# Optimization experiments

Measured on AMD Instinct MI355X. Metric: run time of the kernel, lower is better.

Reference implementation:

```python
import jax, jax.numpy as jnp
import numpy as np

N_NODES = 50000
N_REL = 1000
N_EDGES = 600000
D = 128
DEPTH = 2


def setup_inputs() -> dict:
    key = jax.random.key(0)
    ks = jax.random.split(key, 10)
    features = jax.random.normal(ks[0], (N_NODES, D), dtype=jnp.float32)
    rel_emb = jax.random.normal(ks[1], (N_REL, D), dtype=jnp.float32)
    # edge list: row0 = destination (sorted, matches coalesced sparse layout), row1 = source
    dst = jnp.sort(jax.random.randint(ks[2], (N_EDGES,), 0, N_NODES))
    src = jax.random.randint(ks[3], (N_EDGES,), 0, N_NODES)
    adj = jnp.stack([dst, src]).astype(jnp.int64)
    # one relation entry per triple: r_index[0]=triple id, r_index[1]=relation id
    r_index = jnp.stack([
        jnp.arange(N_EDGES, dtype=jnp.int64),
        jax.random.randint(ks[4], (N_EDGES,), 0, N_REL).astype(jnp.int64),
    ])
    r_val = jax.random.uniform(ks[5], (N_EDGES,), dtype=jnp.float32)
    # Xavier-ish params
    attn_w = jax.random.normal(ks[6], (3 * D, 1), dtype=jnp.float32) * 0.05
    attn_b = jnp.zeros((1,), dtype=jnp.float32)
    gate_w = jax.random.normal(ks[7], (3 * D, 1), dtype=jnp.float32) * 0.05
    gate_b = jnp.zeros((1,), dtype=jnp.float32)
    attn_kernels = jax.random.normal(ks[8], (DEPTH, D, 1), dtype=jnp.float32) * (6.0 / (D + 1)) ** 0.5
    return {"features": features, "rel_emb": rel_emb, "adj": adj, "r_index": r_index,
            "r_val": r_val, "attn_w": attn_w, "attn_b": attn_b, "gate_w": gate_w,
            "gate_b": gate_b, "attn_kernels": attn_kernels}


def _segment_softmax(vals, seg, n):
    # numerically stable softmax over edges grouped by destination node `seg`
    m = jax.ops.segment_max(vals, seg, num_segments=n)
    e = jnp.exp(vals - m[seg])
    s = jax.ops.segment_sum(e, seg, num_segments=n)
    return e / s[seg]


def reference(features, rel_emb, adj, r_index, r_val, attn_w, attn_b, gate_w, gate_b, attn_kernels):
    n_nodes = features.shape[0]
    n_triples = adj.shape[1]
    depth = attn_kernels.shape[0]
    dst, src_idx = adj[0], adj[1]

    feats = jnp.tanh(features)
    outs_c = [feats]
    outs_s = [feats]

    for l in range(depth):
        # sparse [triple, rel] @ rel_emb -> per-triple relation embedding
        tri_rel = jax.ops.segment_sum(r_val[:, None] * rel_emb[r_index[1]], r_index[0],
                                      num_segments=n_triples)  # [E, D]
        tri_rel = tri_rel / jnp.maximum(
            jnp.linalg.norm(tri_rel, axis=1, keepdims=True), 1e-12)
        # gather neighbors and reflect through relation hyperplane
        neighs = feats[src_idx]  # [E, D]
        neighs = neighs - 2.0 * jnp.sum(neighs * tri_rel, axis=1, keepdims=True) * tri_rel
        # structural attention + row-wise sparse softmax
        att_struct = _segment_softmax((tri_rel @ attn_kernels[l])[:, 0], dst, n_nodes)
        feats = jnp.tanh(jax.ops.segment_sum(neighs * att_struct[:, None], dst,
                                             num_segments=n_nodes))
        outs_c.append(feats)
        # semantic branch on updated features
        neighs2 = feats[src_idx]
        source_emb = feats[dst]
        diff_raw = source_emb - neighs2
        att_input = jnp.concatenate([source_emb, neighs2, diff_raw], axis=-1)  # [E, 3D]
        att_score = jnp.maximum(jax.nn.sigmoid(att_input @ attn_w + attn_b)[:, 0], 1e-4)
        gate_score = jax.nn.sigmoid(att_input @ gate_w + gate_b)[:, 0]
        final_att = gate_score * att_score + (1.0 - gate_score) * att_struct
        att = _segment_softmax(final_att, dst, n_nodes)
        new_diff = jnp.tanh(jax.ops.segment_sum(diff_raw * att[:, None], dst,
                                                num_segments=n_nodes))
        outs_s.append(new_diff)

    return (jnp.concatenate(outs_c, axis=-1), jnp.concatenate(outs_s, axis=-1))
```

## Files before the change

kernel.cpp:

```cpp
#include <hip/hip_runtime.h>
#include <math.h>

#define N_NODES 50000
#define N_REL   1000
#define N_EDGES 600000
#define D       128
#define OUT_COLS 384

typedef unsigned short ushortT;

#define FEAT0_BLOCKS  ((N_NODES * (D / 4) + 255) / 256)
#define RELN_BLOCKS   ((N_REL + 3) / 4)
#define ROWPTR_BLOCKS ((N_NODES + 1 + 255) / 256)
#define SETUP_BLOCKS  (FEAT0_BLOCKS + RELN_BLOCKS + ROWPTR_BLOCKS + 1)

__device__ __forceinline__ float wave_reduce_sum64(float v) {
#pragma unroll
    for (int m = 1; m < 64; m <<= 1) v += __shfl_xor(v, m, 64);
    return v;
}

template <int CTRL>
__device__ __forceinline__ float dpp_add_(float v) {
    int t = __builtin_amdgcn_update_dpp(0, __float_as_int(v), CTRL, 0xf, 0xf, true);
    return v + __int_as_float(t);
}
__device__ __forceinline__ float group_sum16(float v) {
    v = dpp_add_<0xB1>(v);
    v = dpp_add_<0x4E>(v);
    v = dpp_add_<0x141>(v);
    v = dpp_add_<0x140>(v);
    return v;
}

__device__ __forceinline__ float tanh_fast(float x) {
    float cx = fminf(fmaxf(x, -20.0f), 20.0f);
    float e = __expf(2.0f * cx);
    return __fdividef(e - 1.0f, e + 1.0f);
}
__device__ __forceinline__ float sigmoid_fast(float x) {
    return __fdividef(1.0f, 1.0f + __expf(-x));
}

__device__ __forceinline__ void bf16x8_to_f32(uint4 q, float4& a, float4& b) {
    a.x = __int_as_float((int)(q.x << 16));
    a.y = __int_as_float((int)(q.x & 0xffff0000u));
    a.z = __int_as_float((int)(q.y << 16));
    a.w = __int_as_float((int)(q.y & 0xffff0000u));
    b.x = __int_as_float((int)(q.z << 16));
    b.y = __int_as_float((int)(q.z & 0xffff0000u));
    b.z = __int_as_float((int)(q.w << 16));
    b.w = __int_as_float((int)(q.w & 0xffff0000u));
}
__device__ __forceinline__ unsigned pack_bf16x2(float lo, float hi) {
    unsigned a = __float_as_uint(lo), b = __float_as_uint(hi);
    a = (a + 0x7fffu + ((a >> 16) & 1u)) >> 16;
    b = (b + 0x7fffu + ((b >> 16) & 1u));
    return (a & 0xffffu) | (b & 0xffff0000u);
}

__global__ __launch_bounds__(256) void k_setup(
        const float* __restrict__ features, const float* __restrict__ rel_emb,
        const float* __restrict__ attn_k, const float* __restrict__ attn_w,
        const float* __restrict__ gate_w, const int* __restrict__ dstv,
        float* __restrict__ out0, float* __restrict__ out1, ushortT* __restrict__ fc0,
        float* __restrict__ rel_norm, float* __restrict__ er0, float* __restrict__ er1,
        float* __restrict__ wcomb, int* __restrict__ row_ptr) {
    int bid = blockIdx.x, tid = threadIdx.x;
    if (bid < FEAT0_BLOCKS) {
        int i = bid * 256 + tid;
        if (i >= N_NODES * (D / 4)) return;
        int n = i >> 5, q = i & 31;
        float4 f = *(const float4*)(features + (size_t)n * D + 4 * q);
        f.x = tanh_fast(f.x); f.y = tanh_fast(f.y);
        f.z = tanh_fast(f.z); f.w = tanh_fast(f.w);
        *(float4*)(out0 + (size_t)n * OUT_COLS + 4 * q) = f;
        *(float4*)(out1 + (size_t)n * OUT_COLS + 4 * q) = f;
        uint2 p = make_uint2(pack_bf16x2(f.x, f.y), pack_bf16x2(f.z, f.w));
        *((uint2*)(fc0 + (size_t)n * D) + q) = p;
    } else if (bid < FEAT0_BLOCKS + RELN_BLOCKS) {
        int wid  = (bid - FEAT0_BLOCKS) * 4 + (tid >> 6);
        int lane = tid & 63;
        if (wid >= N_REL) return;
        float2 v = *(const float2*)(rel_emb + (size_t)wid * D + 2 * lane);
        float sq = wave_reduce_sum64(v.x * v.x + v.y * v.y);
        float inv = 1.0f / fmaxf(sqrtf(sq), 1e-12f);
        float2 u = make_float2(v.x * inv, v.y * inv);
        *(float2*)(rel_norm + (size_t)wid * D + 2 * lane) = u;
        float2 k0 = *(const float2*)(attn_k + 2 * lane);
        float2 k1 = *(const float2*)(attn_k + D + 2 * lane);
        float d0 = wave_reduce_sum64(u.x * k0.x + u.y * k0.y);
        float d1 = wave_reduce_sum64(u.x * k1.x + u.y * k1.y);
        if (lane == 0) { er0[wid] = __expf(d0); er1[wid] = __expf(d1); }
    } else if (bid < FEAT0_BLOCKS + RELN_BLOCKS + ROWPTR_BLOCKS) {
        int n = (bid - FEAT0_BLOCKS - RELN_BLOCKS) * 256 + tid;
        if (n > N_NODES) return;
        int lo = 0, hi = N_EDGES;
        while (lo < hi) {
            int mid = (lo + hi) >> 1;
            if (dstv[mid] < n) lo = mid + 1; else hi = mid;
        }
        row_ptr[n] = lo;
    } else {
        int j = tid;
        if (j >= D) return;
        wcomb[j]         = attn_w[j] + attn_w[2 * D + j];
        wcomb[D + j]     = attn_w[D + j] - attn_w[2 * D + j];
        wcomb[2 * D + j] = gate_w[j] + gate_w[2 * D + j];
        wcomb[3 * D + j] = gate_w[D + j] - gate_w[2 * D + j];
    }
}

__global__ __launch_bounds__(256) void k_struct(
        const ushortT* __restrict__ finC,
        ushortT* __restrict__ foutC,
        float* __restrict__ foutS,
        const int* __restrict__ row_ptr, const int* __restrict__ srcv,
        const int* __restrict__ relv, const float* __restrict__ rval,
        const float* __restrict__ er,
        const float* __restrict__ rel_norm, const float* __restrict__ wcomb,
        float* __restrict__ node_Z, float* __restrict__ proj) {
    int n    = (blockIdx.x * blockDim.x + threadIdx.x) >> 6;
    int lane = threadIdx.x & 63;
    int g = lane >> 4, l = lane & 15;
    if (n >= N_NODES) return;
    int beg = row_ptr[n], end = row_ptr[n + 1];

    float4 acc0 = make_float4(0.f, 0.f, 0.f, 0.f);
    float4 acc1 = make_float4(0.f, 0.f, 0.f, 0.f);
    float Zp = 0.f;

    for (int cs = beg; cs < end; cs += 64) {
        int cnt = min(64, end - cs);
        int my_s = 0, my_r = -1; float my_w = 0.f;
        if (lane < cnt) {
            int e = cs + lane;
            my_s = srcv[e];
            int rr = relv[e];
            bool pos = rval[e] > 0.0f;
            my_r = pos ? rr : -1;
            my_w = pos ? er[rr] : 1.0f;
            Zp += my_w;
        }
        int nit = (cnt + 3) >> 2;
        int   s = __shfl(my_s, g, 64);
        int   r = __shfl(my_r, g, 64);
        float w = __shfl(my_w, g, 64);
        uint4 xq = *((const uint4*)(finC + (size_t)s * D) + l);
        {
            int rr = r < 0 ? 0 : r;
            const float* up = rel_norm + (size_t)rr * D + 8 * l;
            float4 u0 = *(const float4*)up;
            float4 u1 = *(const float4*)(up + 4);
            for (int i = 0; i < nit; ++i) {
                int s_c = s; int r_c = r; float w_c = w;
                uint4 xq_c = xq; float4 u0_c = u0, u1_c = u1;
                (void)s_c;
                if (i + 1 < nit) {
                    int sl2 = ((i + 1) << 2) | g;
                    s = __shfl(my_s, sl2, 64);
                    r = __shfl(my_r, sl2, 64);
                    w = __shfl(my_w, sl2, 64);
                    xq = *((const uint4*)(finC + (size_t)s * D) + l);
                    int rr2 = r < 0 ? 0 : r;
                    const float* up2 = rel_norm + (size_t)rr2 * D + 8 * l;
                    u0 = *(const float4*)up2;
                    u1 = *(const float4*)(up2 + 4);
                }
                float4 x0, x1;
                bf16x8_to_f32(xq_c, x0, x1);
                float p = x0.x*u0_c.x + x0.y*u0_c.y + x0.z*u0_c.z + x0.w*u0_c.w
                        + x1.x*u1_c.x + x1.y*u1_c.y + x1.z*u1_c.z + x1.w*u1_c.w;
                p = group_sum16(p);
                float wc = (r_c >= 0) ? 2.0f * w_c * p : 0.0f;
                acc0.x += w_c * x0.x - wc * u0_c.x;
                acc0.y += w_c * x0.y - wc * u0_c.y;
                acc0.z += w_c * x0.z - wc * u0_c.z;
                acc0.w += w_c * x0.w - wc * u0_c.w;
                acc1.x += w_c * x1.x - wc * u1_c.x;
                acc1.y += w_c * x1.y - wc * u1_c.y;
                acc1.z += w_c * x1.z - wc * u1_c.z;
                acc1.w += w_c * x1.w - wc * u1_c.w;
            }
        }
    }
    float Z = group_sum16(Zp);
    Z += __shfl_xor(Z, 16, 64);
    Z += __shfl_xor(Z, 32, 64);
#pragma unroll
    for (int m = 16; m < 64; m <<= 1) {
        acc0.x += __shfl_xor(acc0.x, m, 64);
        acc0.y += __shfl_xor(acc0.y, m, 64);
        acc0.z += __shfl_xor(acc0.z, m, 64);
        acc0.w += __shfl_xor(acc0.w, m, 64);
        acc1.x += __shfl_xor(acc1.x, m, 64);
        acc1.y += __shfl_xor(acc1.y, m, 64);
        acc1.z += __shfl_xor(acc1.z, m, 64);
        acc1.w += __shfl_xor(acc1.w, m, 64);
    }
    float invZ = (end > beg) ? (1.0f / Z) : 0.0f;
    float4 o0, o1;
    o0.x = tanh_fast(acc0.x * invZ); o0.y = tanh_fast(acc0.y * invZ);
    o0.z = tanh_fast(acc0.z * invZ); o0.w = tanh_fast(acc0.w * invZ);
    o1.x = tanh_fast(acc1.x * invZ); o1.y = tanh_fast(acc1.y * invZ);
    o1.z = tanh_fast(acc1.z * invZ); o1.w = tanh_fast(acc1.w * invZ);

    float pr[4];
#pragma unroll
    for (int k = 0; k < 4; ++k) {
        const float* wp = wcomb + k * D + 8 * l;
        float4 w0 = *(const float4*)wp;
        float4 w1 = *(const float4*)(wp + 4);
        float p = o0.x*w0.x + o0.y*w0.y + o0.z*w0.z + o0.w*w0.w
                + o1.x*w1.x + o1.y*w1.y + o1.z*w1.z + o1.w*w1.w;
        pr[k] = group_sum16(p);
    }
    if (lane == 0) {
        node_Z[n] = Z;
        *(float4*)(proj + 4 * (size_t)n) = make_float4(pr[0], pr[1], pr[2], pr[3]);
    }
    if (g == 0) {
        float* op = foutS + (size_t)n * OUT_COLS + 8 * l;
        *(float4*)op = o0;
        *(float4*)(op + 4) = o1;
        uint4 pk = make_uint4(pack_bf16x2(o0.x, o0.y), pack_bf16x2(o0.z, o0.w),
                              pack_bf16x2(o1.x, o1.y), pack_bf16x2(o1.z, o1.w));
        *((uint4*)(foutC + (size_t)n * D) + l) = pk;
    }
}

__global__ __launch_bounds__(256) void k_sem(
        const ushortT* __restrict__ featsC,
        const float* __restrict__ seF,
        float* __restrict__ oput,
        const int* __restrict__ row_ptr, const int* __restrict__ srcv,
        const int* __restrict__ relv, const float* __restrict__ rval,
        const float* __restrict__ er, const float* __restrict__ node_Z,
        const float* __restrict__ proj,
        const float* __restrict__ attn_b, const float* __restrict__ gate_b) {
    int n    = (blockIdx.x * blockDim.x + threadIdx.x) >> 6;
    int lane = threadIdx.x & 63;
    int g = lane >> 4, l = lane & 15;
    if (n >= N_NODES) return;
    int beg = row_ptr[n], end = row_ptr[n + 1];

    float4 pn = *(const float4*)(proj + 4 * (size_t)n);
    float ca = pn.x + attn_b[0];
    float cg = pn.z + gate_b[0];
    float invZ = (end > beg) ? (1.0f / node_Z[n]) : 0.0f;

    float4 acc0 = make_float4(0.f, 0.f, 0.f, 0.f);
    float4 acc1 = make_float4(0.f, 0.f, 0.f, 0.f);
    float Zs = 0.f;

    for (int cs = beg; cs < end; cs += 64) {
        int cnt = min(64, end - cs);
        int my_s = 0; float my_wt = 0.f;
        if (lane < cnt) {
            int e = cs + lane;
            my_s = srcv[e];
            int rr = relv[e];
            bool pos = rval[e] > 0.0f;
            float sw = (pos ? er[rr] : 1.0f) * invZ;
            float4 ps = *(const float4*)(proj + 4 * (size_t)my_s);
            float as = fmaxf(sigmoid_fast(ca + ps.y), 1e-4f);
            float gt = sigmoid_fast(cg + ps.w);
            my_wt = __expf(gt * as + (1.0f - gt) * sw);
            Zs += my_wt;
        }
        int nit = (cnt + 3) >> 2;
        int   s  = __shfl(my_s, g, 64);
        float wt = __shfl(my_wt, g, 64);
        uint4 xq = *((const uint4*)(featsC + (size_t)s * D) + l);
        for (int i = 0; i < nit; ++i) {
            float wt_c = wt; uint4 xq_c = xq;
            if (i + 1 < nit) {
                int sl2 = ((i + 1) << 2) | g;
                s  = __shfl(my_s, sl2, 64);
                wt = __shfl(my_wt, sl2, 64);
                xq = *((const uint4*)(featsC + (size_t)s * D) + l);
            }
            float4 x0, x1;
            bf16x8_to_f32(xq_c, x0, x1);
            acc0.x += wt_c * x0.x; acc0.y += wt_c * x0.y;
            acc0.z += wt_c * x0.z; acc0.w += wt_c * x0.w;
            acc1.x += wt_c * x1.x; acc1.y += wt_c * x1.y;
            acc1.z += wt_c * x1.z; acc1.w += wt_c * x1.w;
        }
    }
    Zs = group_sum16(Zs);
    Zs += __shfl_xor(Zs, 16, 64);
    Zs += __shfl_xor(Zs, 32, 64);
#pragma unroll
    for (int m = 16; m < 64; m <<= 1) {
        acc0.x += __shfl_xor(acc0.x, m, 64);
        acc0.y += __shfl_xor(acc0.y, m, 64);
        acc0.z += __shfl_xor(acc0.z, m, 64);
        acc0.w += __shfl_xor(acc0.w, m, 64);
        acc1.x += __shfl_xor(acc1.x, m, 64);
        acc1.y += __shfl_xor(acc1.y, m, 64);
        acc1.z += __shfl_xor(acc1.z, m, 64);
        acc1.w += __shfl_xor(acc1.w, m, 64);
    }
    if (g == 0) {
        float invZs = (end > beg) ? (1.0f / Zs) : 0.0f;
        float sc    = (end > beg) ? 1.0f : 0.0f;
        const float* sp = seF + (size_t)n * OUT_COLS + 8 * l;
        float4 s0 = *(const float4*)sp;
        float4 s1 = *(const float4*)(sp + 4);
        float4 o0, o1;
        o0.x = tanh_fast(sc * (s0.x - acc0.x * invZs));
        o0.y = tanh_fast(sc * (s0.y - acc0.y * invZs));
        o0.z = tanh_fast(sc * (s0.z - acc0.z * invZs));
        o0.w = tanh_fast(sc * (s0.w - acc0.w * invZs));
        o1.x = tanh_fast(sc * (s1.x - acc1.x * invZs));
        o1.y = tanh_fast(sc * (s1.y - acc1.y * invZs));
        o1.z = tanh_fast(sc * (s1.z - acc1.z * invZs));
        o1.w = tanh_fast(sc * (s1.w - acc1.w * invZs));
        float* op = oput + (size_t)n * OUT_COLS + 8 * l;
        *(float4*)op = o0;
        *(float4*)(op + 4) = o1;
    }
}

extern "C" void kernel_launch(void* const* d_in, const int* in_sizes, int n_in,
                              void* d_out, int out_size, void* d_ws, size_t ws_size,
                              hipStream_t stream) {
    const float* features = (const float*)d_in[0];
    const float* rel_emb  = (const float*)d_in[1];
    const int*   adj      = (const int*)d_in[2];
    const int*   r_index  = (const int*)d_in[3];
    const float* r_val    = (const float*)d_in[4];
    const float* attn_w   = (const float*)d_in[5];
    const float* attn_b   = (const float*)d_in[6];
    const float* gate_w   = (const float*)d_in[7];
    const float* gate_b   = (const float*)d_in[8];
    const float* attn_k   = (const float*)d_in[9];

    float* out0 = (float*)d_out;
    float* out1 = out0 + (size_t)N_NODES * OUT_COLS;

    float* rel_norm = (float*)d_ws;
    float* er0      = rel_norm + (size_t)N_REL * D;
    float* er1      = er0 + N_REL;
    float* wcomb    = er1 + N_REL;
    float* proj     = wcomb + 4 * D;
    float* node_Z   = proj + 4 * (size_t)N_NODES;
    int*   row_ptr  = (int*)(node_Z + N_NODES);
    ushortT* fc0    = (ushortT*)(row_ptr + N_NODES + 4);
    ushortT* fc1    = fc0 + (size_t)N_NODES * D;
    ushortT* fc2    = fc1 + (size_t)N_NODES * D;

    const int* dstv = adj;
    const int* srcv = adj + N_EDGES;
    const int* relv = r_index + N_EDGES;

    k_setup<<<SETUP_BLOCKS, 256, 0, stream>>>(
        features, rel_emb, attn_k, attn_w, gate_w, dstv,
        out0, out1, fc0, rel_norm, er0, er1, wcomb, row_ptr);

    const ushortT* fcin[3] = {fc0, fc1, fc2};
    for (int l = 0; l < 2; ++l) {
        const float* er = l ? er1 : er0;
        k_struct<<<(N_NODES + 3) / 4, 256, 0, stream>>>(
            fcin[l], (ushortT*)fcin[l + 1], out0 + (size_t)(l + 1) * D,
            row_ptr, srcv, relv, r_val, er, rel_norm, wcomb, node_Z, proj);
        k_sem<<<(N_NODES + 3) / 4, 256, 0, stream>>>(
            fcin[l + 1], out0 + (size_t)(l + 1) * D, out1 + (size_t)(l + 1) * D,
            row_ptr, srcv, relv, r_val, er, node_Z, proj, attn_b, gate_b);
    }
}
```

Before: 376.9 us.

## Fuse layer-0 semantic pass with layer-1 structural pass into one kernel

New measurement: 360.6 us. -4.3%, faster.

```diff
diff --git a/kernel.cpp b/kernel.cpp
--- a/kernel.cpp
+++ b/kernel.cpp
@@ -147,41 +147,38 @@
         int   r = __shfl(my_r, g, 64);
         float w = __shfl(my_w, g, 64);
         uint4 xq = *((const uint4*)(finC + (size_t)s * D) + l);
-        {
-            int rr = r < 0 ? 0 : r;
-            const float* up = rel_norm + (size_t)rr * D + 8 * l;
-            float4 u0 = *(const float4*)up;
-            float4 u1 = *(const float4*)(up + 4);
-            for (int i = 0; i < nit; ++i) {
-                int s_c = s; int r_c = r; float w_c = w;
-                uint4 xq_c = xq; float4 u0_c = u0, u1_c = u1;
-                (void)s_c;
-                if (i + 1 < nit) {
-                    int sl2 = ((i + 1) << 2) | g;
-                    s = __shfl(my_s, sl2, 64);
-                    r = __shfl(my_r, sl2, 64);
-                    w = __shfl(my_w, sl2, 64);
-                    xq = *((const uint4*)(finC + (size_t)s * D) + l);
-                    int rr2 = r < 0 ? 0 : r;
-                    const float* up2 = rel_norm + (size_t)rr2 * D + 8 * l;
-                    u0 = *(const float4*)up2;
-                    u1 = *(const float4*)(up2 + 4);
-                }
-                float4 x0, x1;
-                bf16x8_to_f32(xq_c, x0, x1);
-                float p = x0.x*u0_c.x + x0.y*u0_c.y + x0.z*u0_c.z + x0.w*u0_c.w
-                        + x1.x*u1_c.x + x1.y*u1_c.y + x1.z*u1_c.z + x1.w*u1_c.w;
-                p = group_sum16(p);
-                float wc = (r_c >= 0) ? 2.0f * w_c * p : 0.0f;
-                acc0.x += w_c * x0.x - wc * u0_c.x;
-                acc0.y += w_c * x0.y - wc * u0_c.y;
-                acc0.z += w_c * x0.z - wc * u0_c.z;
-                acc0.w += w_c * x0.w - wc * u0_c.w;
-                acc1.x += w_c * x1.x - wc * u1_c.x;
-                acc1.y += w_c * x1.y - wc * u1_c.y;
-                acc1.z += w_c * x1.z - wc * u1_c.z;
-                acc1.w += w_c * x1.w - wc * u1_c.w;
+        int rr0 = r < 0 ? 0 : r;
+        const float* up = rel_norm + (size_t)rr0 * D + 8 * l;
+        float4 u0 = *(const float4*)up;
+        float4 u1 = *(const float4*)(up + 4);
+        for (int i = 0; i < nit; ++i) {
+            int r_c = r; float w_c = w;
+            uint4 xq_c = xq; float4 u0_c = u0, u1_c = u1;
+            if (i + 1 < nit) {
+                int sl2 = ((i + 1) << 2) | g;
+                s = __shfl(my_s, sl2, 64);
+                r = __shfl(my_r, sl2, 64);
+                w = __shfl(my_w, sl2, 64);
+                xq = *((const uint4*)(finC + (size_t)s * D) + l);
+                int rr2 = r < 0 ? 0 : r;
+                const float* up2 = rel_norm + (size_t)rr2 * D + 8 * l;
+                u0 = *(const float4*)up2;
+                u1 = *(const float4*)(up2 + 4);
             }
+            float4 x0, x1;
+            bf16x8_to_f32(xq_c, x0, x1);
+            float p = x0.x*u0_c.x + x0.y*u0_c.y + x0.z*u0_c.z + x0.w*u0_c.w
+                    + x1.x*u1_c.x + x1.y*u1_c.y + x1.z*u1_c.z + x1.w*u1_c.w;
+            p = group_sum16(p);
+            float wc = (r_c >= 0) ? 2.0f * w_c * p : 0.0f;
+            acc0.x += w_c * x0.x - wc * u0_c.x;
+            acc0.y += w_c * x0.y - wc * u0_c.y;
+            acc0.z += w_c * x0.z - wc * u0_c.z;
+            acc0.w += w_c * x0.w - wc * u0_c.w;
+            acc1.x += w_c * x1.x - wc * u1_c.x;
+            acc1.y += w_c * x1.y - wc * u1_c.y;
+            acc1.z += w_c * x1.z - wc * u1_c.z;
+            acc1.w += w_c * x1.w - wc * u1_c.w;
         }
     }
     float Z = group_sum16(Zp);
@@ -226,6 +223,164 @@
         uint4 pk = make_uint4(pack_bf16x2(o0.x, o0.y), pack_bf16x2(o0.z, o0.w),
                               pack_bf16x2(o1.x, o1.y), pack_bf16x2(o1.z, o1.w));
         *((uint4*)(foutC + (size_t)n * D) + l) = pk;
+    }
+}
+
+__global__ __launch_bounds__(256) void k_fused(
+        const ushortT* __restrict__ finC,
+        const float* __restrict__ seF,
+        ushortT* __restrict__ foutC,
+        float* __restrict__ foutS,
+        float* __restrict__ oputSem,
+        const int* __restrict__ row_ptr, const int* __restrict__ srcv,
+        const int* __restrict__ relv, const float* __restrict__ rval,
+        const float* __restrict__ er_sem,
+        const float* __restrict__ er_st,
+        const float* __restrict__ rel_norm, const float* __restrict__ wcomb,
+        const float* __restrict__ node_Z0, const float* __restrict__ proj0,
+        float* __restrict__ node_Z1, float* __restrict__ proj1,
+        const float* __restrict__ attn_b, const float* __restrict__ gate_b) {
+    int n    = (blockIdx.x * blockDim.x + threadIdx.x) >> 6;
+    int lane = threadIdx.x & 63;
+    int g = lane >> 4, l = lane & 15;
+    if (n >= N_NODES) return;
+    int beg = row_ptr[n], end = row_ptr[n + 1];
+
+    float4 pn = *(const float4*)(proj0 + 4 * (size_t)n);
+    float ca = pn.x + attn_b[0];
+    float cg = pn.z + gate_b[0];
+    float invZ0 = (end > beg) ? (1.0f / node_Z0[n]) : 0.0f;
+
+    float4 st0 = make_float4(0.f, 0.f, 0.f, 0.f);
+    float4 st1 = make_float4(0.f, 0.f, 0.f, 0.f);
+    float4 sm0 = make_float4(0.f, 0.f, 0.f, 0.f);
+    float4 sm1 = make_float4(0.f, 0.f, 0.f, 0.f);
+    float Zp = 0.f, Zs = 0.f;
+
+    for (int cs = beg; cs < end; cs += 64) {
+        int cnt = min(64, end - cs);
+        int my_s = 0, my_r = -1; float my_w = 0.f, my_wt = 0.f;
+        if (lane < cnt) {
+            int e = cs + lane;
+            my_s = srcv[e];
+            int rr = relv[e];
+            bool pos = rval[e] > 0.0f;
+            my_r = pos ? rr : -1;
+            my_w = pos ? er_st[rr] : 1.0f;
+            float sw = (pos ? er_sem[rr] : 1.0f) * invZ0;
+            float4 ps = *(const float4*)(proj0 + 4 * (size_t)my_s);
+            float as = fmaxf(sigmoid_fast(ca + ps.y), 1e-4f);
+            float gt = sigmoid_fast(cg + ps.w);
+            my_wt = __expf(gt * as + (1.0f - gt) * sw);
+            Zp += my_w; Zs += my_wt;
+        }
+        int nit = (cnt + 3) >> 2;
+        int   s  = __shfl(my_s, g, 64);
+        int   r  = __shfl(my_r, g, 64);
+        float w  = __shfl(my_w, g, 64);
+        float wt = __shfl(my_wt, g, 64);
+        uint4 xq = *((const uint4*)(finC + (size_t)s * D) + l);
+        int rr0 = r < 0 ? 0 : r;
+        const float* up = rel_norm + (size_t)rr0 * D + 8 * l;
+        float4 u0 = *(const float4*)up;
+        float4 u1 = *(const float4*)(up + 4);
+        for (int i = 0; i < nit; ++i) {
+            int r_c = r; float w_c = w, wt_c = wt;
+            uint4 xq_c = xq; float4 u0_c = u0, u1_c = u1;
+            if (i + 1 < nit) {
+                int sl2 = ((i + 1) << 2) | g;
+                s  = __shfl(my_s, sl2, 64);
+                r  = __shfl(my_r, sl2, 64);
+                w  = __shfl(my_w, sl2, 64);
+                wt = __shfl(my_wt, sl2, 64);
+                xq = *((const uint4*)(finC + (size_t)s * D) + l);
+                int rr2 = r < 0 ? 0 : r;
+                const float* up2 = rel_norm + (size_t)rr2 * D + 8 * l;
+                u0 = *(const float4*)up2;
+                u1 = *(const float4*)(up2 + 4);
+            }
+            float4 x0, x1;
+            bf16x8_to_f32(xq_c, x0, x1);
+            float p = x0.x*u0_c.x + x0.y*u0_c.y + x0.z*u0_c.z + x0.w*u0_c.w
+                    + x1.x*u1_c.x + x1.y*u1_c.y + x1.z*u1_c.z + x1.w*u1_c.w;
+            p = group_sum16(p);
+            float wc = (r_c >= 0) ? 2.0f * w_c * p : 0.0f;
+            st0.x += w_c * x0.x - wc * u0_c.x;
+            st0.y += w_c * x0.y - wc * u0_c.y;
+            st0.z += w_c * x0.z - wc * u0_c.z;
+            st0.w += w_c * x0.w - wc * u0_c.w;
+            st1.x += w_c * x1.x - wc * u1_c.x;
+            st1.y += w_c * x1.y - wc * u1_c.y;
+            st1.z += w_c * x1.z - wc * u1_c.z;
+            st1.w += w_c * x1.w - wc * u1_c.w;
+            sm0.x += wt_c * x0.x; sm0.y += wt_c * x0.y;
+            sm0.z += wt_c * x0.z; sm0.w += wt_c * x0.w;
+            sm1.x += wt_c * x1.x; sm1.y += wt_c * x1.y;
+            sm1.z += wt_c * x1.z; sm1.w += wt_c * x1.w;
+        }
+    }
+    float Z = group_sum16(Zp);
+    Z += __shfl_xor(Z, 16, 64);
+    Z += __shfl_xor(Z, 32, 64);
+    float ZsT = group_sum16(Zs);
+    ZsT += __shfl_xor(ZsT, 16, 64);
+    ZsT += __shfl_xor(ZsT, 32, 64);
+#pragma unroll
+    for (int m = 16; m < 64; m <<= 1) {
+        st0.x += __shfl_xor(st0.x, m, 64); st0.y += __shfl_xor(st0.y, m, 64);
+        st0.z += __shfl_xor(st0.z, m, 64); st0.w += __shfl_xor(st0.w, m, 64);
+        st1.x += __shfl_xor(st1.x, m, 64); st1.y += __shfl_xor(st1.y, m, 64);
+        st1.z += __shfl_xor(st1.z, m, 64); st1.w += __shfl_xor(st1.w, m, 64);
+        sm0.x += __shfl_xor(sm0.x, m, 64); sm0.y += __shfl_xor(sm0.y, m, 64);
+        sm0.z += __shfl_xor(sm0.z, m, 64); sm0.w += __shfl_xor(sm0.w, m, 64);
+        sm1.x += __shfl_xor(sm1.x, m, 64); sm1.y += __shfl_xor(sm1.y, m, 64);
+        sm1.z += __shfl_xor(sm1.z, m, 64); sm1.w += __shfl_xor(sm1.w, m, 64);
+    }
+    float invZ = (end > beg) ? (1.0f / Z) : 0.0f;
+    float4 o0, o1;
+    o0.x = tanh_fast(st0.x * invZ); o0.y = tanh_fast(st0.y * invZ);
+    o0.z = tanh_fast(st0.z * invZ); o0.w = tanh_fast(st0.w * invZ);
+    o1.x = tanh_fast(st1.x * invZ); o1.y = tanh_fast(st1.y * invZ);
+    o1.z = tanh_fast(st1.z * invZ); o1.w = tanh_fast(st1.w * invZ);
+
+    float pr[4];
+#pragma unroll
+    for (int k = 0; k < 4; ++k) {
+        const float* wp = wcomb + k * D + 8 * l;
+        float4 w0 = *(const float4*)wp;
+        float4 w1 = *(const float4*)(wp + 4);
+        float p = o0.x*w0.x + o0.y*w0.y + o0.z*w0.z + o0.w*w0.w
+                + o1.x*w1.x + o1.y*w1.y + o1.z*w1.z + o1.w*w1.w;
+        pr[k] = group_sum16(p);
+    }
+    if (lane == 0) {
+        node_Z1[n] = Z;
+        *(float4*)(proj1 + 4 * (size_t)n) = make_float4(pr[0], pr[1], pr[2], pr[3]);
+    }
+    if (g == 0) {
+        float* op = foutS + (size_t)n * OUT_COLS + 8 * l;
+        *(float4*)op = o0;
+        *(float4*)(op + 4) = o1;
+        uint4 pk = make_uint4(pack_bf16x2(o0.x, o0.y), pack_bf16x2(o0.z, o0.w),
+                              pack_bf16x2(o1.x, o1.y), pack_bf16x2(o1.z, o1.w));
+        *((uint4*)(foutC + (size_t)n * D) + l) = pk;
+        float invZs = (end > beg) ? (1.0f / ZsT) : 0.0f;
+        float sc    = (end > beg) ? 1.0f : 0.0f;
+        const float* sp = seF + (size_t)n * OUT_COLS + 8 * l;
+        float4 s0 = *(const float4*)sp;
+        float4 s1 = *(const float4*)(sp + 4);
+        float4 q0, q1;
+        q0.x = tanh_fast(sc * (s0.x - sm0.x * invZs));
+        q0.y = tanh_fast(sc * (s0.y - sm0.y * invZs));
+        q0.z = tanh_fast(sc * (s0.z - sm0.z * invZs));
+        q0.w = tanh_fast(sc * (s0.w - sm0.w * invZs));
+        q1.x = tanh_fast(sc * (s1.x - sm1.x * invZs));
+        q1.y = tanh_fast(sc * (s1.y - sm1.y * invZs));
+        q1.z = tanh_fast(sc * (s1.z - sm1.z * invZs));
+        q1.w = tanh_fast(sc * (s1.w - sm1.w * invZs));
+        float* oq = oputSem + (size_t)n * OUT_COLS + 8 * l;
+        *(float4*)oq = q0;
+        *(float4*)(oq + 4) = q1;
     }
 }
 
@@ -344,9 +499,11 @@
     float* er0      = rel_norm + (size_t)N_REL * D;
     float* er1      = er0 + N_REL;
     float* wcomb    = er1 + N_REL;
-    float* proj     = wcomb + 4 * D;
-    float* node_Z   = proj + 4 * (size_t)N_NODES;
-    int*   row_ptr  = (int*)(node_Z + N_NODES);
+    float* proj0    = wcomb + 4 * D;
+    float* proj1    = proj0 + 4 * (size_t)N_NODES;
+    float* node_Z0  = proj1 + 4 * (size_t)N_NODES;
+    float* node_Z1  = node_Z0 + N_NODES;
+    int*   row_ptr  = (int*)(node_Z1 + N_NODES);
     ushortT* fc0    = (ushortT*)(row_ptr + N_NODES + 4);
     ushortT* fc1    = fc0 + (size_t)N_NODES * D;
     ushortT* fc2    = fc1 + (size_t)N_NODES * D;
@@ -359,14 +516,16 @@
         features, rel_emb, attn_k, attn_w, gate_w, dstv,
         out0, out1, fc0, rel_norm, er0, er1, wcomb, row_ptr);
 
-    const ushortT* fcin[3] = {fc0, fc1, fc2};
-    for (int l = 0; l < 2; ++l) {
-        const float* er = l ? er1 : er0;
-        k_struct<<<(N_NODES + 3) / 4, 256, 0, stream>>>(
-            fcin[l], (ushortT*)fcin[l + 1], out0 + (size_t)(l + 1) * D,
-            row_ptr, srcv, relv, r_val, er, rel_norm, wcomb, node_Z, proj);
-        k_sem<<<(N_NODES + 3) / 4, 256, 0, stream>>>(
-            fcin[l + 1], out0 + (size_t)(l + 1) * D, out1 + (size_t)(l + 1) * D,
-            row_ptr, srcv, relv, r_val, er, node_Z, proj, attn_b, gate_b);
-    }
-}
+    k_struct<<<(N_NODES + 3) / 4, 256, 0, stream>>>(
+        fc0, fc1, out0 + (size_t)1 * D,
+        row_ptr, srcv, relv, r_val, er0, rel_norm, wcomb, node_Z0, proj0);
+
+    k_fused<<<(N_NODES + 3) / 4, 256, 0, stream>>>(
+        fc1, out0 + (size_t)1 * D, fc2, out0 + (size_t)2 * D, out1 + (size_t)1 * D,
+        row_ptr, srcv, relv, r_val, er0, er1, rel_norm, wcomb,
+        node_Z0, proj0, node_Z1, proj1, attn_b, gate_b);
+
+    k_sem<<<(N_NODES + 3) / 4, 256, 0, stream>>>(
+        fc2, out0 + (size_t)2 * D, out1 + (size_t)2 * D,
+        row_ptr, srcv, relv, r_val, er1, node_Z1, proj1, attn_b, gate_b);
+}
```
